# Optimization experiments

Hardware: AMD Instinct MI355X
Metric: run time of the kernel (lower is better)

The kernel has to match this reference:

```python
import jax, jax.numpy as jnp
from jax import lax
import numpy as np

B, C, H, W = 8, 256, 64, 64
STRIDE, NH = 2, 8
ED_QK, ED_V = 64, 256  # embed_dim//ratio (divisible by heads), embed_dim
HQ, WQ = H // STRIDE, W // STRIDE
L = HQ * WQ


def conv2d(x, w, b, stride=1, pad=0):
    y = lax.conv_general_dilated(x, w, (stride, stride), ((pad, pad), (pad, pad)),
                                 dimension_numbers=('NCHW', 'OIHW', 'NCHW'))
    return y + b[None, :, None, None]


def setup_inputs() -> dict:
    key = jax.random.key(0)
    ks = jax.random.split(key, 24)
    s = 0.05
    f32 = jnp.float32
    inp = {
        'qkv_pos': jax.random.normal(ks[0], (B, C, H, W), f32),
        'qkv_cha': jax.random.normal(ks[1], (B, C, H, W), f32),
        # POS branch params (standard convs)
        'Wq_pos': jax.random.normal(ks[2], (ED_QK, C, 2, 2), f32) * s,
        'bq_pos': jax.random.normal(ks[3], (ED_QK,), f32) * s,
        'Wk_pos': jax.random.normal(ks[4], (ED_QK, C, 2, 2), f32) * s,
        'bk_pos': jax.random.normal(ks[5], (ED_QK,), f32) * s,
        'Wv_pos': jax.random.normal(ks[6], (ED_V, C, 2, 2), f32) * s,
        'bv_pos': jax.random.normal(ks[7], (ED_V,), f32) * s,
        'Wo_pos': jax.random.normal(ks[8], (C, ED_V, 3, 3), f32) * s,
        'bo_pos': jax.random.normal(ks[9], (C,), f32) * s,
        'gamma_pos': jnp.full((1,), 0.5, f32),
        # CHA branch params (grouped convs, groups=C, 1 in-ch -> NH out-ch per group)
        'Wq_cha': jax.random.normal(ks[10], (C, NH, 2, 2), f32) * s,
        'bq_cha': jax.random.normal(ks[11], (C, NH), f32) * s,
        'Wk_cha': jax.random.normal(ks[12], (C, NH, 2, 2), f32) * s,
        'bk_cha': jax.random.normal(ks[13], (C, NH), f32) * s,
        'Wv_cha': jax.random.normal(ks[14], (C, NH, 2, 2), f32) * s,
        'bv_cha': jax.random.normal(ks[15], (C, NH), f32) * s,
        # grouped ConvTranspose2d (groups=C, NH in-ch per group -> 1 out-ch), k=s=2
        'Wt_cha': jax.random.normal(ks[16], (C, NH, 2, 2), f32) * s,
        'bt_cha': jax.random.normal(ks[17], (C,), f32) * s,
        'gamma_cha': jnp.full((1,), 0.5, f32),
        # fusion conv: concat -> 2C in, C out, 3x3
        'Wf': jax.random.normal(ks[18], (C, 2 * C, 3, 3), f32) * s,
        'bf': jax.random.normal(ks[19], (C,), f32) * s,
    }
    return inp


def _gproj(x, w, b):
    # grouped conv with kernel==stride==2, 1 in-ch per group -> NH out-ch per group
    xp = x.reshape(B, C, HQ, STRIDE, WQ, STRIDE)
    y = jnp.einsum('bgikjl,ghkl->bghij', xp, w) + b[None, :, :, None, None]
    # channel order c = g*NH + h (torch grouped-conv layout); torch then reshapes
    # the flat C*NH channels into (NH, C) -> same as a direct reshape here
    return y.reshape(B, NH, C, L)


def reference(qkv_pos, qkv_cha, Wq_pos, bq_pos, Wk_pos, bk_pos, Wv_pos, bv_pos,
              Wo_pos, bo_pos, gamma_pos, Wq_cha, bq_cha, Wk_cha, bk_cha,
              Wv_cha, bv_cha, Wt_cha, bt_cha, gamma_cha, Wf, bf):
    hd = ED_QK // NH
    # ---- POS (spatial) attention ----
    qp = conv2d(qkv_pos, Wq_pos, bq_pos, STRIDE).reshape(B, NH, hd, L).transpose(0, 1, 3, 2)
    kp = conv2d(qkv_pos, Wk_pos, bk_pos, STRIDE).reshape(B, NH, hd, L).transpose(0, 1, 3, 2)
    vp = conv2d(qkv_pos, Wv_pos, bv_pos, STRIDE).reshape(B, NH, ED_V // NH, L).transpose(0, 1, 3, 2)
    attn_p = jax.nn.softmax(jnp.einsum('bhqd,bhkd->bhqk', qp, kp) * (hd ** -0.5), axis=-1)
    op = jnp.einsum('bhqk,bhkd->bhqd', attn_p, vp).transpose(0, 1, 3, 2).reshape(B, ED_V, HQ, WQ)
    op = conv2d(op, Wo_pos, bo_pos, 1, 1)
    op = jax.image.resize(op, (B, C, H, W), 'bilinear')  # Upsample(align_corners=False)
    out_pos = qkv_pos + op * gamma_pos
    # ---- CHA (channel) attention ----
    qc = _gproj(qkv_cha, Wq_cha, bq_cha)  # [B,NH,C,L]
    kc = _gproj(qkv_cha, Wk_cha, bk_cha)
    vc = _gproj(qkv_cha, Wv_cha, bv_cha)
    attn_c = jax.nn.softmax(jnp.einsum('bhcl,bhdl->bhcd', qc, kc) * (L ** -0.5), axis=-1)
    oc = jnp.einsum('bhcd,bhdl->bhcl', attn_c, vc)  # [B,NH,C,L]
    # flat channel c = h*C + g; grouped ConvTranspose2d groups by c//NH -> reshape (C,NH)
    ocg = oc.reshape(B, C, NH, HQ, WQ)
    oc = jnp.einsum('bgipq,gikl->bgpkql', ocg, Wt_cha).reshape(B, C, H, W) + bt_cha[None, :, None, None]
    out_cha = qkv_cha + oc * gamma_cha
    # ---- fusion: concat (slices are full since slides=0) + 3x3 conv ----
    out = jnp.concatenate([out_pos, out_cha], axis=1)
    return conv2d(out, Wf, bf, 1, 1)
```

## Files before the change

kernel.cpp:

```cpp
#include <hip/hip_runtime.h>
#include <math.h>


typedef __attribute__((ext_vector_type(8))) short bf16x8;
typedef __attribute__((ext_vector_type(4))) float f32x4;

__device__ __forceinline__ ushort f2bf(float f) {
  union { float f; unsigned u; } v; v.f = f;
  unsigned r = (v.u + 0x7FFFu + ((v.u >> 16) & 1u)) >> 16;
  return (ushort)r;
}

template <int CIN>
__global__ __launch_bounds__(256) void k_prepack9(
    const float* __restrict__ W, ushort* __restrict__ out)
{
  const int i = blockIdx.x * 256 + threadIdx.x;
  const int t = i / (256 * CIN);
  const int r = i - t * (256 * CIN);
  const int oc = r / CIN;
  const int c = r - oc * CIN;
  out[i] = f2bf(W[((size_t)oc * CIN + c) * 9 + t]);
}

__global__ __launch_bounds__(256) void k_cast_wqkv(
    const float* __restrict__ Wq, const float* __restrict__ Wk,
    const float* __restrict__ Wv, ushort* __restrict__ out)
{
  const int i = blockIdx.x * 256 + threadIdx.x;
  const int o = i >> 10, k = i & 1023;
  float v;
  if (o < 64)       v = Wq[(size_t)o * 1024 + k];
  else if (o < 128) v = Wk[(size_t)(o - 64) * 1024 + k];
  else              v = Wv[(size_t)(o - 128) * 1024 + k];
  out[i] = f2bf(v);
}

__global__ __launch_bounds__(256) void k_pack_pos(
    const float* __restrict__ x, ushort* __restrict__ Ap)
{
  const int t = blockIdx.x * 256 + threadIdx.x;
  const int j4 = t & 7;
  const int i  = (t >> 3) & 31;
  const int c  = (t >> 8) & 255;
  const int b  = t >> 16;
  const float* xb = x + (((size_t)b * 256 + c) << 12) + (2 * i) * 64 + 8 * j4;
  union { float4 v[2]; float f[8]; } r0, r1;
  r0.v[0] = *(const float4*)(xb);
  r0.v[1] = *(const float4*)(xb + 4);
  r1.v[0] = *(const float4*)(xb + 64);
  r1.v[1] = *(const float4*)(xb + 68);
  #pragma unroll
  for (int jj = 0; jj < 4; ++jj) {
    const int l = i * 32 + j4 * 4 + jj;
    union { ushort u[4]; uint2 d; } pk;
    pk.u[0] = f2bf(r0.f[2 * jj]);
    pk.u[1] = f2bf(r0.f[2 * jj + 1]);
    pk.u[2] = f2bf(r1.f[2 * jj]);
    pk.u[3] = f2bf(r1.f[2 * jj + 1]);
    *(uint2*)(Ap + ((((size_t)b << 10) + l) << 10) + c * 4) = pk.d;
  }
}

__global__ __launch_bounds__(256) void k_pos_qkv_mfma(
    const ushort* __restrict__ Ap, const ushort* __restrict__ Wqkv,
    const float* __restrict__ bq, const float* __restrict__ bk,
    const float* __restrict__ bv,
    ushort* __restrict__ Qb, ushort* __restrict__ Kb, ushort* __restrict__ Vtb)
{
  const int n0 = blockIdx.x * 128, oc0 = blockIdx.y * 128, b = blockIdx.z;
  const int tid = threadIdx.x, lane = tid & 63, w = tid >> 6;
  __shared__ ushort As[128][32], Bs[128][32];
  const ushort* Abw = Wqkv + (size_t)oc0 * 1024;
  const ushort* Bb  = Ap + (((size_t)b << 10) + n0) * 1024;
  const int wr = w >> 1, wc = w & 1;
  f32x4 acc[4][4];
  #pragma unroll
  for (int mi = 0; mi < 4; ++mi)
    #pragma unroll
    for (int ni = 0; ni < 4; ++ni) {
      f32x4 z = {0.f, 0.f, 0.f, 0.f};
      acc[mi][ni] = z;
    }
  for (int kc = 0; kc < 1024; kc += 32) {
    __syncthreads();
    #pragma unroll
    for (int q = 0; q < 2; ++q) {
      int idx = w * 128 + q * 64 + lane;
      int row = idx >> 2, seg = idx & 3;
      const ushort* srcA = Abw + (size_t)row * 1024 + kc + seg * 8;
      const ushort* srcB = Bb + (size_t)row * 1024 + kc + seg * 8;
      char* dstA = (char*)&As[0][0] + w * 2048 + q * 1024;
      char* dstB = (char*)&Bs[0][0] + w * 2048 + q * 1024;
      __builtin_amdgcn_global_load_lds(
          (const __attribute__((address_space(1))) unsigned*)srcA,
          (__attribute__((address_space(3))) unsigned*)dstA, 16, 0, 0);
      __builtin_amdgcn_global_load_lds(
          (const __attribute__((address_space(1))) unsigned*)srcB,
          (__attribute__((address_space(3))) unsigned*)dstB, 16, 0, 0);
    }
    __syncthreads();
    bf16x8 af[4], bfv[4];
    #pragma unroll
    for (int mi = 0; mi < 4; ++mi)
      af[mi] = *(const bf16x8*)&As[wr * 64 + mi * 16 + (lane & 15)][(lane >> 4) * 8];
    #pragma unroll
    for (int ni = 0; ni < 4; ++ni)
      bfv[ni] = *(const bf16x8*)&Bs[wc * 64 + ni * 16 + (lane & 15)][(lane >> 4) * 8];
    #pragma unroll
    for (int mi = 0; mi < 4; ++mi)
      #pragma unroll
      for (int ni = 0; ni < 4; ++ni)
        acc[mi][ni] = __builtin_amdgcn_mfma_f32_16x16x32_bf16(
            af[mi], bfv[ni], acc[mi][ni], 0, 0, 0);
  }
  #pragma unroll
  for (int mi = 0; mi < 4; ++mi) {
    const int oc = oc0 + wr * 64 + mi * 16 + (lane >> 4) * 4;
    if (oc >= 384) continue;
    if (oc < 64) {
      const int hh = oc >> 3, e = oc & 7;
      float4 bb = *(const float4*)(bq + oc);
      #pragma unroll
      for (int ni = 0; ni < 4; ++ni) {
        const int l = n0 + wc * 64 + ni * 16 + (lane & 15);
        union { ushort u[4]; uint2 d; } pk;
        pk.u[0] = f2bf((acc[mi][ni][0] + bb.x) * 0.35355339059327373f);
        pk.u[1] = f2bf((acc[mi][ni][1] + bb.y) * 0.35355339059327373f);
        pk.u[2] = f2bf((acc[mi][ni][2] + bb.z) * 0.35355339059327373f);
        pk.u[3] = f2bf((acc[mi][ni][3] + bb.w) * 0.35355339059327373f);
        *(uint2*)(Qb + (((((size_t)b * 8 + hh) << 10) + l) << 5) + e) = pk.d;
      }
    } else if (oc < 128) {
      const int o2 = oc - 64, hh = o2 >> 3, e = o2 & 7;
      float4 bb = *(const float4*)(bk + o2);
      #pragma unroll
      for (int ni = 0; ni < 4; ++ni) {
        const int l = n0 + wc * 64 + ni * 16 + (lane & 15);
        union { ushort u[4]; uint2 d; } pk;
        pk.u[0] = f2bf(acc[mi][ni][0] + bb.x);
        pk.u[1] = f2bf(acc[mi][ni][1] + bb.y);
        pk.u[2] = f2bf(acc[mi][ni][2] + bb.z);
        pk.u[3] = f2bf(acc[mi][ni][3] + bb.w);
        *(uint2*)(Kb + (((((size_t)b * 8 + hh) << 10) + l) << 5) + e) = pk.d;
      }
    } else {
      const int o2 = oc - 128, hh = o2 >> 5, dd = o2 & 31;
      float4 bb = *(const float4*)(bv + o2);
      #pragma unroll
      for (int ni = 0; ni < 4; ++ni) {
        const int l = n0 + wc * 64 + ni * 16 + (lane & 15);
        ushort* vb = Vtb + ((((size_t)b * 8 + hh) * 32 + dd) << 10) + l;
        vb[0]      = f2bf(acc[mi][ni][0] + bb.x);
        vb[1024]   = f2bf(acc[mi][ni][1] + bb.y);
        vb[2048]   = f2bf(acc[mi][ni][2] + bb.z);
        vb[3072]   = f2bf(acc[mi][ni][3] + bb.w);
      }
    }
  }
}

__global__ __launch_bounds__(256) void k_pos_flash(
    const ushort* __restrict__ Qb, const ushort* __restrict__ Kb,
    const ushort* __restrict__ Vtb, ushort* __restrict__ op_pad)
{
  const int qt = blockIdx.x, h = blockIdx.y, b = blockIdx.z;
  const int bh = b * 8 + h;
  const int tid = threadIdx.x, lane = tid & 63, wq = tid >> 6;
  const int c = lane & 15, g = lane >> 4;
  __shared__ __align__(16) ushort Ps[4][32][72];
  const int qbase = qt * 128 + wq * 32;
  bf16x8 qf[2];
  #pragma unroll
  for (int nt = 0; nt < 2; ++nt)
    qf[nt] = *(const bf16x8*)(Qb + (((size_t)bh << 10) + qbase + nt * 16 + c) * 32 + g * 8);
  f32x4 o[2][2];
  #pragma unroll
  for (int mt = 0; mt < 2; ++mt)
    #pragma unroll
    for (int nt = 0; nt < 2; ++nt) {
      f32x4 z = {0.f, 0.f, 0.f, 0.f};
      o[mt][nt] = z;
    }
  float m[2] = {-1e30f, -1e30f}, l[2] = {0.f, 0.f};
  const ushort* Kbh = Kb + ((size_t)bh << 15);
  const ushort* Vbh = Vtb + ((size_t)bh << 15);

  for (int kt = 0; kt < 16; ++kt) {
    const int kb0 = kt * 64;
    bf16x8 kf[4];
    #pragma unroll
    for (int mt = 0; mt < 4; ++mt)
      kf[mt] = *(const bf16x8*)(Kbh + (size_t)(kb0 + mt * 16 + c) * 32 + g * 8);
    f32x4 s[4][2];
    #pragma unroll
    for (int mt = 0; mt < 4; ++mt)
      #pragma unroll
      for (int nt = 0; nt < 2; ++nt) {
        f32x4 z = {0.f, 0.f, 0.f, 0.f};
        s[mt][nt] = __builtin_amdgcn_mfma_f32_16x16x32_bf16(kf[mt], qf[nt], z, 0, 0, 0);
      }
    #pragma unroll
    for (int nt = 0; nt < 2; ++nt) {
      float tmax = -1e30f;
      #pragma unroll
      for (int mt = 0; mt < 4; ++mt)
        #pragma unroll
        for (int r = 0; r < 4; ++r)
          tmax = fmaxf(tmax, s[mt][nt][r]);
      tmax = fmaxf(tmax, __shfl_xor(tmax, 16, 64));
      tmax = fmaxf(tmax, __shfl_xor(tmax, 32, 64));
      const float mn = fmaxf(m[nt], tmax);
      const float alpha = __expf(m[nt] - mn);
      m[nt] = mn;
      float rs = 0.f;
      #pragma unroll
      for (int mt = 0; mt < 4; ++mt) {
        union { ushort u[4]; uint2 d; } pk;
        #pragma unroll
        for (int r = 0; r < 4; ++r) {
          float p = __expf(s[mt][nt][r] - mn);
          rs += p;
          pk.u[r] = f2bf(p);
        }
        *(uint2*)&Ps[wq][nt * 16 + c][mt * 16 + g * 4] = pk.d;
      }
      rs += __shfl_xor(rs, 16, 64);
      rs += __shfl_xor(rs, 32, 64);
      l[nt] = l[nt] * alpha + rs;
      #pragma unroll
      for (int mt = 0; mt < 2; ++mt)
        #pragma unroll
        for (int r = 0; r < 4; ++r)
          o[mt][nt][r] *= alpha;
    }
    #pragma unroll
    for (int kc = 0; kc < 2; ++kc) {
      bf16x8 vf[2], pf[2];
      #pragma unroll
      for (int mt = 0; mt < 2; ++mt)
        vf[mt] = *(const bf16x8*)(Vbh + (size_t)(mt * 16 + c) * 1024 + kb0 + kc * 32 + g * 8);
      #pragma unroll
      for (int nt = 0; nt < 2; ++nt)
        pf[nt] = *(const bf16x8*)&Ps[wq][nt * 16 + c][kc * 32 + g * 8];
      #pragma unroll
      for (int mt = 0; mt < 2; ++mt)
        #pragma unroll
        for (int nt = 0; nt < 2; ++nt)
          o[mt][nt] = __builtin_amdgcn_mfma_f32_16x16x32_bf16(vf[mt], pf[nt], o[mt][nt], 0, 0, 0);
    }
  }
  #pragma unroll
  for (int nt = 0; nt < 2; ++nt) {
    const float linv = 1.f / l[nt];
    const int q = qbase + nt * 16 + c;
    const int y = q >> 5, x = q & 31;
    ushort* dst = op_pad + ((size_t)b * 1156 + (y + 1) * 34 + (x + 1)) * 256 + h * 32;
    #pragma unroll
    for (int mt = 0; mt < 2; ++mt) {
      union { ushort u[4]; uint2 d; } pk;
      #pragma unroll
      for (int r = 0; r < 4; ++r)
        pk.u[r] = f2bf(o[mt][nt][r] * linv);
      *(uint2*)(dst + mt * 16 + g * 4) = pk.d;
    }
  }
}

template <int CIN, int S, int PW, int OUT_NHWC>
__global__ __launch_bounds__(256) void k_conv9_mfma(
    const ushort* __restrict__ in, const ushort* __restrict__ W9,
    const float* __restrict__ bias, float* __restrict__ out)
{
  const int n0 = blockIdx.x * 128, oc0 = blockIdx.y * 128, b = blockIdx.z;
  const int tid = threadIdx.x, lane = tid & 63, w = tid >> 6;
  __shared__ ushort As[128][32], Bs[128][32];
  const int wr = w >> 1, wc = w & 1;
  f32x4 acc[4][4];
  #pragma unroll
  for (int mi = 0; mi < 4; ++mi)
    #pragma unroll
    for (int ni = 0; ni < 4; ++ni) {
      f32x4 z = {0.f, 0.f, 0.f, 0.f};
      acc[mi][ni] = z;
    }
  int rowq[2], segq[2], basep[2];
  #pragma unroll
  for (int q = 0; q < 2; ++q) {
    int idx = w * 128 + q * 64 + lane;
    rowq[q] = idx >> 2;
    segq[q] = (idx & 3) * 8;
    int n = n0 + rowq[q];
    int y = n / S, x = n % S;
    basep[q] = y * PW + x;
  }
  const ushort* inb = in + (size_t)b * (PW * PW) * CIN;

  for (int t = 0; t < 9; ++t) {
    const int offp = (t / 3) * PW + (t % 3);
    const ushort* wt = W9 + (size_t)t * 256 * CIN;
    for (int kc = 0; kc < CIN; kc += 32) {
      __syncthreads();
      #pragma unroll
      for (int q = 0; q < 2; ++q) {
        const ushort* srcA = wt + (size_t)(oc0 + rowq[q]) * CIN + kc + segq[q];
        const ushort* srcB = inb + (size_t)(basep[q] + offp) * CIN + kc + segq[q];
        char* dstA = (char*)&As[0][0] + w * 2048 + q * 1024;
        char* dstB = (char*)&Bs[0][0] + w * 2048 + q * 1024;
        __builtin_amdgcn_global_load_lds(
            (const __attribute__((address_space(1))) unsigned*)srcA,
            (__attribute__((address_space(3))) unsigned*)dstA, 16, 0, 0);
        __builtin_amdgcn_global_load_lds(
            (const __attribute__((address_space(1))) unsigned*)srcB,
            (__attribute__((address_space(3))) unsigned*)dstB, 16, 0, 0);
      }
      __syncthreads();
      bf16x8 af[4], bfv[4];
      #pragma unroll
      for (int mi = 0; mi < 4; ++mi)
        af[mi] = *(const bf16x8*)&As[wr * 64 + mi * 16 + (lane & 15)][(lane >> 4) * 8];
      #pragma unroll
      for (int ni = 0; ni < 4; ++ni)
        bfv[ni] = *(const bf16x8*)&Bs[wc * 64 + ni * 16 + (lane & 15)][(lane >> 4) * 8];
      #pragma unroll
      for (int mi = 0; mi < 4; ++mi)
        #pragma unroll
        for (int ni = 0; ni < 4; ++ni)
          acc[mi][ni] = __builtin_amdgcn_mfma_f32_16x16x32_bf16(
              af[mi], bfv[ni], acc[mi][ni], 0, 0, 0);
    }
  }
  if (OUT_NHWC) {
    float* outb = out + (size_t)b * (S * S) * 256;
    #pragma unroll
    for (int mi = 0; mi < 4; ++mi) {
      const int oc = oc0 + wr * 64 + mi * 16 + (lane >> 4) * 4;
      float4 bb = *(const float4*)(bias + oc);
      #pragma unroll
      for (int ni = 0; ni < 4; ++ni) {
        const int n = n0 + wc * 64 + ni * 16 + (lane & 15);
        float4 v;
        v.x = acc[mi][ni][0] + bb.x;
        v.y = acc[mi][ni][1] + bb.y;
        v.z = acc[mi][ni][2] + bb.z;
        v.w = acc[mi][ni][3] + bb.w;
        *(float4*)(outb + (size_t)n * 256 + oc) = v;
      }
    }
  } else {
    float* outb = out + (size_t)b * 256 * (S * S);
    #pragma unroll
    for (int mi = 0; mi < 4; ++mi) {
      #pragma unroll
      for (int r = 0; r < 4; ++r) {
        int oc = oc0 + wr * 64 + mi * 16 + (lane >> 4) * 4 + r;
        float bb = bias[oc];
        #pragma unroll
        for (int ni = 0; ni < 4; ++ni) {
          int n = n0 + wc * 64 + ni * 16 + (lane & 15);
          outb[(size_t)oc * (S * S) + n] = acc[mi][ni][r] + bb;
        }
      }
    }
  }
}

#define STAGE_CONV(s_, bi_)                                                    \
  {                                                                            \
    const int t_ = (s_) >> 3, kc_ = ((s_) & 7) << 6;                           \
    const ushort* wt_ = W9 + t_ * 131072 + kc_;                                \
    const ushort* ib_ = inb + ((t_ / 3) * 66 + (t_ % 3)) * 512 + kc_;          \
    _Pragma("unroll")                                                          \
    for (int q_ = 0; q_ < 2; ++q_) {                                           \
      __builtin_amdgcn_global_load_lds(                                        \
          (const __attribute__((address_space(1))) unsigned*)(wt_ + aInv[q_]), \
          (__attribute__((address_space(3))) unsigned*)                        \
              ((char*)lds + (bi_) * 16384 + (w * 16 + q_ * 8) * 128),          \
          16, 0, 0);                                                           \
    }                                                                          \
    _Pragma("unroll")                                                          \
    for (int q_ = 0; q_ < 4; ++q_) {                                           \
      __builtin_amdgcn_global_load_lds(                                        \
          (const __attribute__((address_space(1))) unsigned*)(ib_ + bInv[q_]), \
          (__attribute__((address_space(3))) unsigned*)                        \
              ((char*)lds + 49152 + (bi_) * 32768 + (w * 32 + q_ * 8) * 128),  \
          16, 0, 0);                                                           \
    }                                                                          \
  }

__global__ __launch_bounds__(512, 2) void k_conv9_pipe(
    const ushort* __restrict__ in, const ushort* __restrict__ W9,
    const float* __restrict__ bias, float* __restrict__ out)
{
  const int n0 = blockIdx.x * 256, oc0 = blockIdx.y * 128, b = blockIdx.z;
  const int tid = threadIdx.x, lane = tid & 63, w = tid >> 6;
  const int wm = w >> 2, wn = w & 3;
  const int g = lane >> 4, c = lane & 15;
  __shared__ __align__(16) ushort lds[73728];
  const ushort* inb = in + (size_t)b * 4356 * 512;

  const int l8 = lane >> 3, lx = lane & 7;
  int aInv[2], bInv[4];
  #pragma unroll
  for (int q = 0; q < 2; ++q) {
    const int row = w * 16 + q * 8 + l8;
    const int cx = (((lx << 4) ^ ((row & 7) << 4)) >> 1);
    aInv[q] = (oc0 + row) * 512 + cx;
  }
  #pragma unroll
  for (int q = 0; q < 4; ++q) {
    const int row = w * 32 + q * 8 + l8;
    const int n = n0 + row;
    const int y = n >> 6, x = n & 63;
    const int cx = (((lx << 4) ^ ((row & 7) << 4)) >> 1);
    bInv[q] = (y * 66 + x) * 512 + cx;
  }

  f32x4 acc[4][4];
  #pragma unroll
  for (int mi = 0; mi < 4; ++mi)
    #pragma unroll
    for (int ni = 0; ni < 4; ++ni) {
      f32x4 z = {0.f, 0.f, 0.f, 0.f};
      acc[mi][ni] = z;
    }

  STAGE_CONV(0, 0);
  STAGE_CONV(1, 1);

  int bi = 0;
  for (int s = 0; s < 72; ++s) {
    if (s < 71) asm volatile("s_waitcnt vmcnt(6)" ::: "memory");
    else        asm volatile("s_waitcnt vmcnt(0)" ::: "memory");
    __builtin_amdgcn_s_barrier();

    const ushort* As  = lds + bi * 8192;
    const ushort* Bsl = lds + 24576 + bi * 16384;
    bf16x8 af[4][2], bfv[4][2];
    #pragma unroll
    for (int mi = 0; mi < 4; ++mi) {
      const int row = wm * 64 + mi * 16 + c;
      const int sx = (row & 7) << 3;
      #pragma unroll
      for (int kh = 0; kh < 2; ++kh)
        af[mi][kh] = *(const bf16x8*)(As + row * 64 + ((kh * 32 + g * 8) ^ sx));
    }
    #pragma unroll
    for (int ni = 0; ni < 4; ++ni) {
      const int row = wn * 64 + ni * 16 + c;
      const int sx = (row & 7) << 3;
      #pragma unroll
      for (int kh = 0; kh < 2; ++kh)
        bfv[ni][kh] = *(const bf16x8*)(Bsl + row * 64 + ((kh * 32 + g * 8) ^ sx));
    }
    int bi2 = bi + 2; if (bi2 >= 3) bi2 -= 3;
    if (s < 70) STAGE_CONV(s + 2, bi2);

    __builtin_amdgcn_s_setprio(1);
    #pragma unroll
    for (int mi = 0; mi < 4; ++mi)
      #pragma unroll
      for (int ni = 0; ni < 4; ++ni) {
        acc[mi][ni] = __builtin_amdgcn_mfma_f32_16x16x32_bf16(
            af[mi][0], bfv[ni][0], acc[mi][ni], 0, 0, 0);
        acc[mi][ni] = __builtin_amdgcn_mfma_f32_16x16x32_bf16(
            af[mi][1], bfv[ni][1], acc[mi][ni], 0, 0, 0);
      }
    __builtin_amdgcn_s_setprio(0);
    ++bi; if (bi == 3) bi = 0;
  }

  float* outb = out + (size_t)b * 1048576;
  #pragma unroll
  for (int mi = 0; mi < 4; ++mi) {
    const int oc = oc0 + wm * 64 + mi * 16 + g * 4;
    float4 bb = *(const float4*)(bias + oc);
    #pragma unroll
    for (int ni = 0; ni < 4; ++ni) {
      const int n = n0 + wn * 64 + ni * 16 + c;
      outb[(size_t)(oc + 0) * 4096 + n] = acc[mi][ni][0] + bb.x;
      outb[(size_t)(oc + 1) * 4096 + n] = acc[mi][ni][1] + bb.y;
      outb[(size_t)(oc + 2) * 4096 + n] = acc[mi][ni][2] + bb.z;
      outb[(size_t)(oc + 3) * 4096 + n] = acc[mi][ni][3] + bb.w;
    }
  }
}

__global__ __launch_bounds__(256) void k_upsample_nhwc(
    const float* __restrict__ xpos, const float* __restrict__ opc,
    const float* __restrict__ gamma, ushort* __restrict__ fused)
{
  const int t = blockIdx.x * 256 + threadIdx.x;
  const int c = (t & 63) * 4;
  const int pix = (t >> 6) & 4095;
  const int b = t >> 18;
  const int y = pix >> 6, xx = pix & 63;
  const int my = y >> 1;
  const int y0 = (y & 1) ? my : my - 1;
  const float fy = (y & 1) ? 0.25f : 0.75f;
  const int mx = xx >> 1;
  const int x0 = (xx & 1) ? mx : mx - 1;
  const float fx = (xx & 1) ? 0.25f : 0.75f;
  const int y0c = max(y0, 0), y1c = min(y0 + 1, 31);
  const int x0c = max(x0, 0), x1c = min(x0 + 1, 31);
  const float* base = opc + (size_t)b * 1024 * 256 + c;
  float4 v00 = *(const float4*)(base + (size_t)(y0c * 32 + x0c) * 256);
  float4 v01 = *(const float4*)(base + (size_t)(y0c * 32 + x1c) * 256);
  float4 v10 = *(const float4*)(base + (size_t)(y1c * 32 + x0c) * 256);
  float4 v11 = *(const float4*)(base + (size_t)(y1c * 32 + x1c) * 256);
  const float w00 = (1.f - fy) * (1.f - fx), w01 = (1.f - fy) * fx;
  const float w10 = fy * (1.f - fx), w11 = fy * fx;
  const float g = gamma[0];
  const float* xr = xpos + ((size_t)b * 256 + c) * 4096 + pix;
  union { ushort u[4]; uint2 q; } o;
  o.u[0] = f2bf(xr[0]          + g * (w00 * v00.x + w01 * v01.x + w10 * v10.x + w11 * v11.x));
  o.u[1] = f2bf(xr[4096]       + g * (w00 * v00.y + w01 * v01.y + w10 * v10.y + w11 * v11.y));
  o.u[2] = f2bf(xr[2 * 4096]   + g * (w00 * v00.z + w01 * v01.z + w10 * v10.z + w11 * v11.z));
  o.u[3] = f2bf(xr[3 * 4096]   + g * (w00 * v00.w + w01 * v01.w + w10 * v10.w + w11 * v11.w));
  *(uint2*)(fused + ((size_t)b * 4356 + (y + 1) * 66 + (xx + 1)) * 512 + c) = o.q;
}

__global__ __launch_bounds__(256) void k_cha_proj(
    const float* __restrict__ x,
    const float* __restrict__ Wq, const float* __restrict__ bq,
    const float* __restrict__ Wk, const float* __restrict__ bk,
    const float* __restrict__ Wv, const float* __restrict__ bv,
    ushort* __restrict__ Qc, ushort* __restrict__ Kc, ushort* __restrict__ Vt)
{
  const int t = blockIdx.x * 256 + threadIdx.x;
  const int bl = t >> 16;
  const int g  = (t >> 8) & 255;
  const int lq = t & 255;
  const int i = lq >> 3, j4 = (lq & 7) << 2;
  const float* xb = x + (((size_t)bl * 256 + g) << 12) + (2 * i) * 64 + 2 * j4;
  union { float4 v[2]; float f[8]; } xr0, xr1;
  xr0.v[0] = *(const float4*)(xb);
  xr0.v[1] = *(const float4*)(xb + 4);
  xr1.v[0] = *(const float4*)(xb + 64);
  xr1.v[1] = *(const float4*)(xb + 68);
  const int bhl = bl * 8 + (g >> 5);
  const int c2b = (g & 31) * 8;
  const int l0 = i * 32 + j4;
  #pragma unroll
  for (int h = 0; h < 8; ++h) {
    float4 w4 = *(const float4*)(Wq + g * 32 + h * 4);
    float bb = bq[g * 8 + h];
    union { ushort u[4]; uint2 q; } o;
    #pragma unroll
    for (int jj = 0; jj < 4; ++jj) {
      float v = xr0.f[2 * jj] * w4.x + xr0.f[2 * jj + 1] * w4.y
              + xr1.f[2 * jj] * w4.z + xr1.f[2 * jj + 1] * w4.w + bb;
      o.u[jj] = f2bf(v * 0.03125f);
    }
    *(uint2*)(Qc + (((size_t)bhl * 256 + c2b + h) << 10) + l0) = o.q;
  }
  #pragma unroll
  for (int h = 0; h < 8; ++h) {
    float4 w4 = *(const float4*)(Wk + g * 32 + h * 4);
    float bb = bk[g * 8 + h];
    union { ushort u[4]; uint2 q; } o;
    #pragma unroll
    for (int jj = 0; jj < 4; ++jj) {
      float v = xr0.f[2 * jj] * w4.x + xr0.f[2 * jj + 1] * w4.y
              + xr1.f[2 * jj] * w4.z + xr1.f[2 * jj + 1] * w4.w + bb;
      o.u[jj] = f2bf(v);
    }
    *(uint2*)(Kc + (((size_t)bhl * 256 + c2b + h) << 10) + l0) = o.q;
  }
  ushort vo[4][8];
  #pragma unroll
  for (int h = 0; h < 8; ++h) {
    float4 w4 = *(const float4*)(Wv + g * 32 + h * 4);
    float bb = bv[g * 8 + h];
    #pragma unroll
    for (int jj = 0; jj < 4; ++jj) {
      float v = xr0.f[2 * jj] * w4.x + xr0.f[2 * jj + 1] * w4.y
              + xr1.f[2 * jj] * w4.z + xr1.f[2 * jj + 1] * w4.w + bb;
      vo[jj][h] = f2bf(v);
    }
  }
  #pragma unroll
  for (int jj = 0; jj < 4; ++jj)
    *(uint4*)(Vt + ((size_t)bhl << 18) + (size_t)(l0 + jj) * 256 + c2b) =
        *(uint4*)&vo[jj][0];
}

__global__ __launch_bounds__(256) void k_cha_scores_mfma(
    const ushort* __restrict__ Qc, const ushort* __restrict__ Kc,
    float* __restrict__ S)
{
  const int c0 = blockIdx.x * 128, d0 = blockIdx.y * 128, bhl = blockIdx.z;
  const int tid = threadIdx.x, lane = tid & 63, w = tid >> 6;
  __shared__ ushort As[128][32], Bs[128][32];
  const ushort* Ab = Qc + ((size_t)bhl * 256 + c0) * 1024;
  const ushort* Bb = Kc + ((size_t)bhl * 256 + d0) * 1024;
  const int wr = w >> 1, wc = w & 1;
  f32x4 acc[4][4];
  #pragma unroll
  for (int mi = 0; mi < 4; ++mi)
    #pragma unroll
    for (int ni = 0; ni < 4; ++ni) {
      f32x4 z = {0.f, 0.f, 0.f, 0.f};
      acc[mi][ni] = z;
    }
  for (int kc = 0; kc < 1024; kc += 32) {
    __syncthreads();
    #pragma unroll
    for (int q = 0; q < 2; ++q) {
      int idx = w * 128 + q * 64 + lane;
      int row = idx >> 2, seg = idx & 3;
      const ushort* srcA = Ab + (size_t)row * 1024 + kc + seg * 8;
      const ushort* srcB = Bb + (size_t)row * 1024 + kc + seg * 8;
      char* dstA = (char*)&As[0][0] + w * 2048 + q * 1024;
      char* dstB = (char*)&Bs[0][0] + w * 2048 + q * 1024;
      __builtin_amdgcn_global_load_lds(
          (const __attribute__((address_space(1))) unsigned*)srcA,
          (__attribute__((address_space(3))) unsigned*)dstA, 16, 0, 0);
      __builtin_amdgcn_global_load_lds(
          (const __attribute__((address_space(1))) unsigned*)srcB,
          (__attribute__((address_space(3))) unsigned*)dstB, 16, 0, 0);
    }
    __syncthreads();
    bf16x8 af[4], bfv[4];
    #pragma unroll
    for (int mi = 0; mi < 4; ++mi)
      af[mi] = *(const bf16x8*)&As[wr * 64 + mi * 16 + (lane & 15)][(lane >> 4) * 8];
    #pragma unroll
    for (int ni = 0; ni < 4; ++ni)
      bfv[ni] = *(const bf16x8*)&Bs[wc * 64 + ni * 16 + (lane & 15)][(lane >> 4) * 8];
    #pragma unroll
    for (int mi = 0; mi < 4; ++mi)
      #pragma unroll
      for (int ni = 0; ni < 4; ++ni)
        acc[mi][ni] = __builtin_amdgcn_mfma_f32_16x16x32_bf16(
            af[mi], bfv[ni], acc[mi][ni], 0, 0, 0);
  }
  float* Sb = S + ((size_t)bhl << 16);
  #pragma unroll
  for (int mi = 0; mi < 4; ++mi)
    #pragma unroll
    for (int r = 0; r < 4; ++r) {
      int c = c0 + wr * 64 + mi * 16 + (lane >> 4) * 4 + r;
      #pragma unroll
      for (int ni = 0; ni < 4; ++ni) {
        int d = d0 + wc * 64 + ni * 16 + (lane & 15);
        Sb[(size_t)c * 256 + d] = acc[mi][ni][r];
      }
    }
}

__global__ __launch_bounds__(256) void k_softmax_p(
    const float* __restrict__ S, ushort* __restrict__ P)
{
  const int row = blockIdx.x * 4 + (threadIdx.x >> 6);
  const int lane = threadIdx.x & 63;
  const float* r = S + (size_t)row * 256;
  float4 v = *(const float4*)(r + lane * 4);
  float m = fmaxf(fmaxf(v.x, v.y), fmaxf(v.z, v.w));
  #pragma unroll
  for (int off = 32; off; off >>= 1) m = fmaxf(m, __shfl_xor(m, off, 64));
  v.x = __expf(v.x - m); v.y = __expf(v.y - m);
  v.z = __expf(v.z - m); v.w = __expf(v.w - m);
  float s = v.x + v.y + v.z + v.w;
  #pragma unroll
  for (int off = 32; off; off >>= 1) s += __shfl_xor(s, off, 64);
  const float inv = 1.f / s;
  union { ushort u[4]; uint2 q; } o;
  o.u[0] = f2bf(v.x * inv); o.u[1] = f2bf(v.y * inv);
  o.u[2] = f2bf(v.z * inv); o.u[3] = f2bf(v.w * inv);
  *(uint2*)(P + (size_t)row * 256 + lane * 4) = o.q;
}

__global__ __launch_bounds__(256) void k_cha_pv(
    const ushort* __restrict__ P, const ushort* __restrict__ Vt,
    const float* __restrict__ x,
    const float* __restrict__ Wt, const float* __restrict__ bt,
    const float* __restrict__ gamma, ushort* __restrict__ fused, int bbase)
{
  const int n0 = blockIdx.x * 128, c0 = blockIdx.y * 128, bhl = blockIdx.z;
  const int b = bbase + (bhl >> 3), h = bhl & 7;
  const int tid = threadIdx.x, lane = tid & 63, w = tid >> 6;
  __shared__ ushort As[128][32], Bs[128][32];
  __shared__ ushort Ot[512][16];
  __shared__ float wt_s[16][32];
  __shared__ float bt_s[16];
  const int gp_base = h * 32 + (c0 >> 3);
  {
    int e = tid;
    wt_s[e >> 5][e & 31] = Wt[(size_t)gp_base * 32 + e];
    e += 256;
    wt_s[e >> 5][e & 31] = Wt[(size_t)gp_base * 32 + e];
    if (tid < 16) bt_s[tid] = bt[gp_base + tid];
  }
  const ushort* Ab = P + (((size_t)bhl << 8) + c0) * 256;
  const ushort* Bb = Vt + ((size_t)bhl << 18) + (size_t)n0 * 256;
  const int wr = w >> 1, wc = w & 1;
  f32x4 acc[4][4];
  #pragma unroll
  for (int mi = 0; mi < 4; ++mi)
    #pragma unroll
    for (int ni = 0; ni < 4; ++ni) {
      f32x4 z = {0.f, 0.f, 0.f, 0.f};
      acc[mi][ni] = z;
    }
  for (int kc = 0; kc < 256; kc += 32) {
    __syncthreads();
    #pragma unroll
    for (int q = 0; q < 2; ++q) {
      int idx = w * 128 + q * 64 + lane;
      int row = idx >> 2, seg = idx & 3;
      const ushort* srcA = Ab + (size_t)row * 256 + kc + seg * 8;
      const ushort* srcB = Bb + (size_t)row * 256 + kc + seg * 8;
      char* dstA = (char*)&As[0][0] + w * 2048 + q * 1024;
      char* dstB = (char*)&Bs[0][0] + w * 2048 + q * 1024;
      __builtin_amdgcn_global_load_lds(
          (const __attribute__((address_space(1))) unsigned*)srcA,
          (__attribute__((address_space(3))) unsigned*)dstA, 16, 0, 0);
      __builtin_amdgcn_global_load_lds(
          (const __attribute__((address_space(1))) unsigned*)srcB,
          (__attribute__((address_space(3))) unsigned*)dstB, 16, 0, 0);
    }
    __syncthreads();
    bf16x8 af[4], bfv[4];
    #pragma unroll
    for (int mi = 0; mi < 4; ++mi)
      af[mi] = *(const bf16x8*)&As[wr * 64 + mi * 16 + (lane & 15)][(lane >> 4) * 8];
    #pragma unroll
    for (int ni = 0; ni < 4; ++ni)
      bfv[ni] = *(const bf16x8*)&Bs[wc * 64 + ni * 16 + (lane & 15)][(lane >> 4) * 8];
    #pragma unroll
    for (int mi = 0; mi < 4; ++mi)
      #pragma unroll
      for (int ni = 0; ni < 4; ++ni)
        acc[mi][ni] = __builtin_amdgcn_mfma_f32_16x16x32_bf16(
            af[mi], bfv[ni], acc[mi][ni], 0, 0, 0);
  }
  const float gm = gamma[0];
  const int col = lane & 15, q = lane >> 4;
  #pragma unroll
  for (int mi = 0; mi < 4; ++mi) {
    const int gloc = wr * 8 + mi * 2 + (q >> 1);
    const int gp = gp_base + gloc;
    const float btv = bt_s[gloc];
    #pragma unroll
    for (int ni = 0; ni < 4; ++ni) {
      float pa[4] = {0.f, 0.f, 0.f, 0.f};
      #pragma unroll
      for (int r = 0; r < 4; ++r) {
        const int i2 = (q & 1) * 4 + r;
        const float a = acc[mi][ni][r];
        pa[0] += a * wt_s[gloc][i2 * 4 + 0];
        pa[1] += a * wt_s[gloc][i2 * 4 + 1];
        pa[2] += a * wt_s[gloc][i2 * 4 + 2];
        pa[3] += a * wt_s[gloc][i2 * 4 + 3];
      }
      float v0 = pa[0] + __shfl_xor(pa[0], 16, 64);
      float v1 = pa[1] + __shfl_xor(pa[1], 16, 64);
      float v2 = pa[2] + __shfl_xor(pa[2], 16, 64);
      float v3 = pa[3] + __shfl_xor(pa[3], 16, 64);
      const int lloc = wc * 64 + ni * 16 + col;
      const int l = n0 + lloc;
      const int p = l >> 5, j = l & 31;
      const int y = 2 * p + (q & 1);
      const float va = (q & 1) ? v2 : v0;
      const float vb = (q & 1) ? v3 : v1;
      const float* xc = x + (((size_t)b * 256 + gp) << 12) + (y << 6) + 2 * j;
      const int lp = (lloc << 2) + (q & 1) * 2;
      Ot[lp][gloc]     = f2bf(xc[0] + gm * (va + btv));
      Ot[lp + 1][gloc] = f2bf(xc[1] + gm * (vb + btv));
    }
  }
  __syncthreads();
  #pragma unroll
  for (int pp2 = 0; pp2 < 2; ++pp2) {
    const int pixl = tid * 2 + pp2;
    const int lloc = pixl >> 2;
    const int l = n0 + lloc;
    const int p = l >> 5, j = l & 31;
    const int yy = 2 * p + ((pixl >> 1) & 1) + 1;
    const int xx = 2 * j + (pixl & 1) + 1;
    const uint4* src = (const uint4*)&Ot[pixl][0];
    uint4* dst = (uint4*)(fused + ((size_t)b * 4356 + yy * 66 + xx) * 512 + 256 + gp_base);
    dst[0] = src[0];
    dst[1] = src[1];
  }
}

extern "C" void kernel_launch(void* const* d_in, const int* in_sizes, int n_in,
                              void* d_out, int out_size, void* d_ws, size_t ws_size,
                              hipStream_t stream)
{
  (void)in_sizes; (void)n_in; (void)out_size; (void)ws_size;
  const float* qkv_pos   = (const float*)d_in[0];
  const float* qkv_cha   = (const float*)d_in[1];
  const float* Wq_pos    = (const float*)d_in[2];
  const float* bq_pos    = (const float*)d_in[3];
  const float* Wk_pos    = (const float*)d_in[4];
  const float* bk_pos    = (const float*)d_in[5];
  const float* Wv_pos    = (const float*)d_in[6];
  const float* bv_pos    = (const float*)d_in[7];
  const float* Wo_pos    = (const float*)d_in[8];
  const float* bo_pos    = (const float*)d_in[9];
  const float* gamma_pos = (const float*)d_in[10];
  const float* Wq_cha    = (const float*)d_in[11];
  const float* bq_cha    = (const float*)d_in[12];
  const float* Wk_cha    = (const float*)d_in[13];
  const float* bk_cha    = (const float*)d_in[14];
  const float* Wv_cha    = (const float*)d_in[15];
  const float* bv_cha    = (const float*)d_in[16];
  const float* Wt_cha    = (const float*)d_in[17];
  const float* bt_cha    = (const float*)d_in[18];
  const float* gamma_cha = (const float*)d_in[19];
  const float* Wf        = (const float*)d_in[20];
  const float* bf        = (const float*)d_in[21];
  float* out = (float*)d_out;

  float* ws = (float*)d_ws;
  ushort* Wpf9    = (ushort*)ws;
  ushort* Wpo9    = (ushort*)(ws + 589824);
  ushort* Qb      = (ushort*)(ws + 884736);
  ushort* Kb      = (ushort*)(ws + 1933312);
  ushort* Vtb     = (ushort*)(ws + 2981888);
  ushort* op_pad  = (ushort*)(ws + 4030464);
  float*  op_conv = ws + 5214208;
  ushort* Ap      = (ushort*)(ws + 7311360);
  ushort* qcb     = (ushort*)(ws + 884736);
  ushort* kcb     = (ushort*)(ws + 5079040);
  ushort* vcT     = (ushort*)(ws + 9273344);
  float*  attn_c  = ws + 13467648;
  ushort* Pb      = (ushort*)(ws + 15564800);
  ushort* fusedb  = (ushort*)(ws + 16613376);
  ushort* Wqkvp   = (ushort*)(ws + 25534464);

  hipMemsetAsync(op_pad, 0, (size_t)2367488 * 2, stream);
  hipMemsetAsync(fusedb, 0, (size_t)17842176 * 2, stream);
  hipMemsetAsync(Qb, 0, (size_t)2097152 * 2, stream);
  k_prepack9<512><<<dim3(4608), 256, 0, stream>>>(Wf, Wpf9);
  k_prepack9<256><<<dim3(2304), 256, 0, stream>>>(Wo_pos, Wpo9);
  k_cast_wqkv<<<dim3(1536), 256, 0, stream>>>(Wq_pos, Wk_pos, Wv_pos, Wqkvp);
  k_pack_pos<<<dim3(2048), 256, 0, stream>>>(qkv_pos, Ap);
  k_pos_qkv_mfma<<<dim3(8, 3, 8), 256, 0, stream>>>(Ap, Wqkvp,
      bq_pos, bk_pos, bv_pos, Qb, Kb, Vtb);
  k_pos_flash<<<dim3(8, 8, 8), 256, 0, stream>>>(Qb, Kb, Vtb, op_pad);
  k_conv9_mfma<256, 32, 34, 1><<<dim3(8, 2, 8), 256, 0, stream>>>(
      op_pad, Wpo9, bo_pos, op_conv);
  k_upsample_nhwc<<<dim3(8192), 256, 0, stream>>>(qkv_pos, op_conv, gamma_pos, fusedb);
  for (int half = 0; half < 2; ++half) {
    const float* xh = qkv_cha + (size_t)half * 4 * 256 * 4096;
    k_cha_proj<<<dim3(1024), 256, 0, stream>>>(xh, Wq_cha, bq_cha,
        Wk_cha, bk_cha, Wv_cha, bv_cha, qcb, kcb, vcT);
    k_cha_scores_mfma<<<dim3(2, 2, 32), 256, 0, stream>>>(qcb, kcb, attn_c);
    k_softmax_p<<<dim3(2048), 256, 0, stream>>>(attn_c, Pb);
    k_cha_pv<<<dim3(8, 2, 32), 256, 0, stream>>>(Pb, vcT, qkv_cha,
        Wt_cha, bt_cha, gamma_cha, fusedb, half * 4);
  }
  k_conv9_pipe<<<dim3(16, 2, 8), 512, 0, stream>>>(fusedb, Wpf9, bf, out);
}
```

Measured before the change: 555.7 us.

## Double-buffer register fragments in conv9 pipeline to overlap LDS reads with MFMA

Restructures the 3x3 conv GEMM main loop so the LDS fragment reads for step s+1 are issued while the MFMAs for step s run, using two sets of register fragments in an unrolled even/odd loop. It also stages three K-slices up front and precomputes the swizzled LDS offsets once. The intent is to hide LDS latency behind matrix-core work. In exchange it doubles fragment register use under a 512-thread, 2-blocks-per-SM launch bound, which risks spills or lower occupancy, and the hand-placed waitcnts and barriers must be exactly right for the 3-buffer ring.

```diff
diff --git a/kernel.cpp b/kernel.cpp
--- a/kernel.cpp
+++ b/kernel.cpp
@@ -388,6 +388,45 @@
     }                                                                          \
   }
 
+#define READ_FRAGS(rb_, AF_, BF_)                                              \
+  {                                                                            \
+    const ushort* As_ = lds + (rb_) * 8192 + (wm * 64 + c) * 64;               \
+    const ushort* Bs_ = lds + 24576 + (rb_) * 16384 + (wn * 64 + c) * 64;      \
+    _Pragma("unroll")                                                          \
+    for (int mi_ = 0; mi_ < 4; ++mi_) {                                        \
+      AF_[mi_][0] = *(const bf16x8*)(As_ + mi_ * 1024 + okh0);                 \
+      AF_[mi_][1] = *(const bf16x8*)(As_ + mi_ * 1024 + okh1);                 \
+    }                                                                          \
+    _Pragma("unroll")                                                          \
+    for (int ni_ = 0; ni_ < 4; ++ni_) {                                        \
+      BF_[ni_][0] = *(const bf16x8*)(Bs_ + ni_ * 1024 + okh0);                 \
+      BF_[ni_][1] = *(const bf16x8*)(Bs_ + ni_ * 1024 + okh1);                 \
+    }                                                                          \
+  }
+
+#define MFMA_SET(AF_, BF_)                                                     \
+  {                                                                            \
+    __builtin_amdgcn_s_setprio(1);                                             \
+    _Pragma("unroll")                                                          \
+    for (int mi_ = 0; mi_ < 4; ++mi_)                                          \
+      _Pragma("unroll")                                                        \
+      for (int ni_ = 0; ni_ < 4; ++ni_) {                                      \
+        acc[mi_][ni_] = __builtin_amdgcn_mfma_f32_16x16x32_bf16(               \
+            AF_[mi_][0], BF_[ni_][0], acc[mi_][ni_], 0, 0, 0);                 \
+        acc[mi_][ni_] = __builtin_amdgcn_mfma_f32_16x16x32_bf16(               \
+            AF_[mi_][1], BF_[ni_][1], acc[mi_][ni_], 0, 0, 0);                 \
+      }                                                                        \
+    __builtin_amdgcn_s_setprio(0);                                             \
+  }
+
+#define PHASE_END(vm_)                                                         \
+  {                                                                            \
+    asm volatile("s_waitcnt lgkmcnt(0)" ::: "memory");                         \
+    asm volatile("s_waitcnt vmcnt(" #vm_ ")" ::: "memory");                    \
+    __builtin_amdgcn_sched_barrier(0);                                         \
+    __builtin_amdgcn_s_barrier();                                              \
+  }
+
 __global__ __launch_bounds__(512, 2) void k_conv9_pipe(
     const ushort* __restrict__ in, const ushort* __restrict__ W9,
     const float* __restrict__ bias, float* __restrict__ out)
@@ -416,6 +455,10 @@
     bInv[q] = (y * 66 + x) * 512 + cx;
   }
 
+  const int sx = (c & 7) << 3;
+  const int okh0 = (g * 8) ^ sx;
+  const int okh1 = (32 + g * 8) ^ sx;
+
   f32x4 acc[4][4];
   #pragma unroll
   for (int mi = 0; mi < 4; ++mi)
@@ -425,50 +468,45 @@
       acc[mi][ni] = z;
     }
 
+  bf16x8 afE[4][2], bfE[4][2], afO[4][2], bfO[4][2];
+
   STAGE_CONV(0, 0);
   STAGE_CONV(1, 1);
-
-  int bi = 0;
-  for (int s = 0; s < 72; ++s) {
-    if (s < 71) asm volatile("s_waitcnt vmcnt(6)" ::: "memory");
-    else        asm volatile("s_waitcnt vmcnt(0)" ::: "memory");
-    __builtin_amdgcn_s_barrier();
-
-    const ushort* As  = lds + bi * 8192;
-    const ushort* Bsl = lds + 24576 + bi * 16384;
-    bf16x8 af[4][2], bfv[4][2];
-    #pragma unroll
-    for (int mi = 0; mi < 4; ++mi) {
-      const int row = wm * 64 + mi * 16 + c;
-      const int sx = (row & 7) << 3;
-      #pragma unroll
-      for (int kh = 0; kh < 2; ++kh)
-        af[mi][kh] = *(const bf16x8*)(As + row * 64 + ((kh * 32 + g * 8) ^ sx));
-    }
-    #pragma unroll
-    for (int ni = 0; ni < 4; ++ni) {
-      const int row = wn * 64 + ni * 16 + c;
-      const int sx = (row & 7) << 3;
-      #pragma unroll
-      for (int kh = 0; kh < 2; ++kh)
-        bfv[ni][kh] = *(const bf16x8*)(Bsl + row * 64 + ((kh * 32 + g * 8) ^ sx));
-    }
-    int bi2 = bi + 2; if (bi2 >= 3) bi2 -= 3;
-    if (s < 70) STAGE_CONV(s + 2, bi2);
-
-    __builtin_amdgcn_s_setprio(1);
-    #pragma unroll
-    for (int mi = 0; mi < 4; ++mi)
-      #pragma unroll
-      for (int ni = 0; ni < 4; ++ni) {
-        acc[mi][ni] = __builtin_amdgcn_mfma_f32_16x16x32_bf16(
-            af[mi][0], bfv[ni][0], acc[mi][ni], 0, 0, 0);
-        acc[mi][ni] = __builtin_amdgcn_mfma_f32_16x16x32_bf16(
-            af[mi][1], bfv[ni][1], acc[mi][ni], 0, 0, 0);
-      }
-    __builtin_amdgcn_s_setprio(0);
-    ++bi; if (bi == 3) bi = 0;
-  }
+  STAGE_CONV(2, 2);
+  asm volatile("s_waitcnt vmcnt(12)" ::: "memory");
+  __builtin_amdgcn_sched_barrier(0);
+  __builtin_amdgcn_s_barrier();
+  READ_FRAGS(0, afE, bfE);
+  PHASE_END(6);
+
+  int rb = 1;
+  for (int p = 0; p < 68; p += 2) {
+    READ_FRAGS(rb, afO, bfO);
+    { int sb = rb + 2; if (sb >= 3) sb -= 3; STAGE_CONV(p + 3, sb); }
+    MFMA_SET(afE, bfE);
+    PHASE_END(6);
+    ++rb; if (rb == 3) rb = 0;
+    READ_FRAGS(rb, afE, bfE);
+    { int sb = rb + 2; if (sb >= 3) sb -= 3; STAGE_CONV(p + 4, sb); }
+    MFMA_SET(afO, bfO);
+    PHASE_END(6);
+    ++rb; if (rb == 3) rb = 0;
+  }
+  READ_FRAGS(rb, afO, bfO);
+  { int sb = rb + 2; if (sb >= 3) sb -= 3; STAGE_CONV(71, sb); }
+  MFMA_SET(afE, bfE);
+  PHASE_END(6);
+  ++rb; if (rb == 3) rb = 0;
+  READ_FRAGS(rb, afE, bfE);
+  MFMA_SET(afO, bfO);
+  PHASE_END(0);
+  ++rb; if (rb == 3) rb = 0;
+  READ_FRAGS(rb, afO, bfO);
+  MFMA_SET(afE, bfE);
+  asm volatile("s_waitcnt lgkmcnt(0)" ::: "memory");
+  __builtin_amdgcn_sched_barrier(0);
+  __builtin_amdgcn_s_barrier();
+  MFMA_SET(afO, bfO);
 
   float* outb = out + (size_t)b * 1048576;
   #pragma unroll
```

Measured after the change: 549.8 us. About the same (-1.1%).
